# Performance work log

Hardware: AMD Instinct MI355X
Metric: run time of the kernel (lower is better)

The kernel has to match this reference:

```python
import jax, jax.numpy as jnp
import numpy as np


def setup_inputs() -> dict:
    key = jax.random.key(0)
    kq, kk, kv = jax.random.split(key, 3)
    B, S, D = 16, 2048, 128
    q = jax.random.normal(kq, (B, S, D), dtype=jnp.float32)
    k = jax.random.normal(kk, (B, S, D), dtype=jnp.float32)
    v = jax.random.normal(kv, (B, S, D), dtype=jnp.float32)
    return {"q": q, "k": k, "v": v}


def reference(q, k, v):
    # scores = q @ k^T * scale  (scale = 1/sqrt(head_dim), the standard value
    # passed to this module; dropout=0.0 and attn_mask=None per defaults)
    scale = q.shape[-1] ** -0.5
    scores = jnp.einsum('bqd,bkd->bqk', q, k) * scale  # [B, S, S]
    attention = jax.nn.softmax(scores, axis=-1)
    context = jnp.einsum('bqk,bkd->bqd', attention, v)  # [B, S, D]
    return (context, attention)
```

## Files before the change

kernel.cpp:

```cpp
#include <hip/hip_runtime.h>

#define SS 2048
#define DD 128
#define NB 16
#define TM 128
#define TN 64
#define NITER (SS / TN)
#define SCALE 0.08838834764831845f

typedef short bf16x8 __attribute__((ext_vector_type(8)));
typedef float f32x4 __attribute__((ext_vector_type(4)));

#define KSTRIDE 136
#define VSTRIDE 72
#define PSTRIDE 72

__device__ __forceinline__ unsigned short f2bf(float x) {
    unsigned u = __builtin_bit_cast(unsigned, x);
    u += 0x7fffu + ((u >> 16) & 1u);
    return (unsigned short)(u >> 16);
}
__device__ __forceinline__ float bf2f(unsigned short h) {
    unsigned u = ((unsigned)h) << 16;
    return __builtin_bit_cast(float, u);
}

__global__ void cvt_qk_kernel(const float* __restrict__ q, const float* __restrict__ k,
                              unsigned short* __restrict__ qb, unsigned short* __restrict__ kb) {
    int i = (blockIdx.x * 256 + threadIdx.x) * 4;
    float4 a = *(const float4*)(q + i);
    float4 b = *(const float4*)(k + i);
    ushort4 ua; ua.x = f2bf(a.x); ua.y = f2bf(a.y); ua.z = f2bf(a.z); ua.w = f2bf(a.w);
    ushort4 ub; ub.x = f2bf(b.x); ub.y = f2bf(b.y); ub.z = f2bf(b.z); ub.w = f2bf(b.w);
    *(ushort4*)(qb + i) = ua;
    *(ushort4*)(kb + i) = ub;
}

__global__ void tr_v_kernel(const float* __restrict__ v, unsigned short* __restrict__ vt) {
    __shared__ unsigned short t[64 * 72];
    int b = blockIdx.z, sb = blockIdx.y * 64, db = blockIdx.x * 64;
    int tid = threadIdx.x;
    int r16 = tid >> 4, c4 = (tid & 15) * 4;
    for (int i = 0; i < 4; ++i) {
        int sl = i * 16 + r16;
        float4 x = *(const float4*)(v + ((size_t)(b * SS + sb + sl) * DD + db + c4));
        ushort4 u; u.x = f2bf(x.x); u.y = f2bf(x.y); u.z = f2bf(x.z); u.w = f2bf(x.w);
        *(ushort4*)&t[sl * 72 + c4] = u;
    }
    __syncthreads();
    for (int i = 0; i < 4; ++i) {
        int dl = i * 16 + r16;
        ushort4 u;
        u.x = t[(c4 + 0) * 72 + dl];
        u.y = t[(c4 + 1) * 72 + dl];
        u.z = t[(c4 + 2) * 72 + dl];
        u.w = t[(c4 + 3) * 72 + dl];
        *(ushort4*)(vt + ((size_t)(b * DD + db + dl) * SS + sb + c4)) = u;
    }
}

__global__ __launch_bounds__(512, 2)
void attn_kernel(const unsigned short* __restrict__ qb,
                 const unsigned short* __restrict__ kb,
                 const unsigned short* __restrict__ vt,
                 float* __restrict__ attn, float* __restrict__ ctx) {
    __shared__ unsigned short K_lds[TN * KSTRIDE];
    __shared__ unsigned short V_lds[DD * VSTRIDE];
    __shared__ unsigned short P_lds[TM * PSTRIDE];
    __shared__ float rs_lds[TM];
    __shared__ float inv_lds[TM];

    const int tid = threadIdx.x;
    const int lane = tid & 63, w = tid >> 6;
    const int wm = w >> 2, wn = w & 3;
    const int l15 = lane & 15, quad = lane >> 4;
    const int bb = blockIdx.y;
    const int q0 = blockIdx.x * TM;

    if (tid < TM) rs_lds[tid] = 0.0f;

    bf16x8 qf[4][4];
    {
        const unsigned short* qg = qb + ((size_t)(bb * SS + q0 + wm * 64 + l15)) * DD + quad * 8;
        for (int mi = 0; mi < 4; ++mi)
            for (int kk = 0; kk < 4; ++kk)
                qf[mi][kk] = *(const bf16x8*)(qg + mi * 16 * DD + kk * 32);
    }

    const unsigned short* kgb = kb + (size_t)bb * SS * DD;
    const unsigned short* vgb = vt + (size_t)bb * DD * SS;

    float rs[16];
    for (int j = 0; j < 16; ++j) rs[j] = 0.0f;

    for (int it = 0; it < NITER; ++it) {
        const int k0 = it * TN;
        __syncthreads();
        {
            const unsigned short* kg = kgb + (size_t)k0 * DD;
            for (int c = 0; c < 2; ++c) {
                int e = c * 4096 + tid * 8;
                *(bf16x8*)&K_lds[(e >> 7) * KSTRIDE + (e & 127)] = *(const bf16x8*)(kg + e);
            }
        }
        __syncthreads();
        f32x4 acc[4];
        for (int mi = 0; mi < 4; ++mi) acc[mi] = (f32x4){0.f, 0.f, 0.f, 0.f};
        for (int kk = 0; kk < 4; ++kk) {
            bf16x8 bf = *(const bf16x8*)&K_lds[(wn * 16 + l15) * KSTRIDE + kk * 32 + quad * 8];
            for (int mi = 0; mi < 4; ++mi)
                acc[mi] = __builtin_amdgcn_mfma_f32_16x16x32_bf16(qf[mi][kk], bf, acc[mi], 0, 0, 0);
        }
        for (int mi = 0; mi < 4; ++mi)
            for (int r = 0; r < 4; ++r)
                rs[mi * 4 + r] += __expf(acc[mi][r] * SCALE);
    }

    for (int j = 0; j < 16; ++j) {
        float v = rs[j];
        v += __shfl_xor(v, 1, 64);
        v += __shfl_xor(v, 2, 64);
        v += __shfl_xor(v, 4, 64);
        v += __shfl_xor(v, 8, 64);
        rs[j] = v;
    }
    if (l15 == 0)
        for (int mi = 0; mi < 4; ++mi)
            for (int r = 0; r < 4; ++r)
                atomicAdd(&rs_lds[wm * 64 + mi * 16 + quad * 4 + r], rs[mi * 4 + r]);
    __syncthreads();
    if (tid < TM) inv_lds[tid] = 1.0f / rs_lds[tid];
    __syncthreads();
    float inv[16];
    for (int mi = 0; mi < 4; ++mi)
        for (int r = 0; r < 4; ++r)
            inv[mi * 4 + r] = inv_lds[wm * 64 + mi * 16 + quad * 4 + r];

    f32x4 cacc[4][2];
    for (int mi = 0; mi < 4; ++mi)
        for (int ni = 0; ni < 2; ++ni) cacc[mi][ni] = (f32x4){0.f, 0.f, 0.f, 0.f};

    float* ag = attn + (size_t)bb * SS * SS + (size_t)q0 * SS;

    for (int it = 0; it < NITER; ++it) {
        const int k0 = it * TN;
        __syncthreads();
        {
            const unsigned short* kg = kgb + (size_t)k0 * DD;
            for (int c = 0; c < 2; ++c) {
                int e = c * 4096 + tid * 8;
                *(bf16x8*)&K_lds[(e >> 7) * KSTRIDE + (e & 127)] = *(const bf16x8*)(kg + e);
            }
        }
        {
            const unsigned short* vg = vgb + k0;
            for (int c = 0; c < 2; ++c) {
                int e = c * 4096 + tid * 8;
                int dr = e >> 6, ck = e & 63;
                *(bf16x8*)&V_lds[dr * VSTRIDE + ck] = *(const bf16x8*)(vg + (size_t)dr * SS + ck);
            }
        }
        __syncthreads();

        f32x4 acc[4];
        for (int mi = 0; mi < 4; ++mi) acc[mi] = (f32x4){0.f, 0.f, 0.f, 0.f};
        for (int kk = 0; kk < 4; ++kk) {
            bf16x8 bf = *(const bf16x8*)&K_lds[(wn * 16 + l15) * KSTRIDE + kk * 32 + quad * 8];
            for (int mi = 0; mi < 4; ++mi)
                acc[mi] = __builtin_amdgcn_mfma_f32_16x16x32_bf16(qf[mi][kk], bf, acc[mi], 0, 0, 0);
        }
        for (int mi = 0; mi < 4; ++mi)
            for (int r = 0; r < 4; ++r) {
                float p = __expf(acc[mi][r] * SCALE) * inv[mi * 4 + r];
                P_lds[(wm * 64 + mi * 16 + quad * 4 + r) * PSTRIDE + wn * 16 + l15] = f2bf(p);
            }
        __syncthreads();

        for (int kk = 0; kk < 2; ++kk) {
            bf16x8 af[4];
            for (int mi = 0; mi < 4; ++mi)
                af[mi] = *(const bf16x8*)&P_lds[(wm * 64 + mi * 16 + l15) * PSTRIDE + kk * 32 + quad * 8];
            for (int ni = 0; ni < 2; ++ni) {
                bf16x8 bf = *(const bf16x8*)&V_lds[((w & 3) * 32 + ni * 16 + l15) * VSTRIDE + kk * 32 + quad * 8];
                for (int mi = 0; mi < 4; ++mi)
                    cacc[mi][ni] = __builtin_amdgcn_mfma_f32_16x16x32_bf16(af[mi], bf, cacc[mi][ni], 0, 0, 0);
            }
        }

        for (int c = 0; c < 4; ++c) {
            int e = c * 2048 + tid * 4;
            int row = e >> 6, col = e & 63;
            const unsigned short* ps = &P_lds[row * PSTRIDE + col];
            float4 o;
            o.x = bf2f(ps[0]); o.y = bf2f(ps[1]); o.z = bf2f(ps[2]); o.w = bf2f(ps[3]);
            *(float4*)(ag + (size_t)row * SS + k0 + col) = o;
        }
    }

    float* cg = ctx + ((size_t)(bb * SS) + q0) * DD;
    for (int mi = 0; mi < 4; ++mi)
        for (int ni = 0; ni < 2; ++ni)
            for (int r = 0; r < 4; ++r) {
                int row = wm * 64 + mi * 16 + quad * 4 + r;
                int col = (w & 3) * 32 + ni * 16 + l15;
                cg[(size_t)row * DD + col] = cacc[mi][ni][r];
            }
}

extern "C" void kernel_launch(void* const* d_in, const int* in_sizes, int n_in,
                              void* d_out, int out_size, void* d_ws, size_t ws_size,
                              hipStream_t stream) {
    const float* q = (const float*)d_in[0];
    const float* k = (const float*)d_in[1];
    const float* v = (const float*)d_in[2];
    float* ctx = (float*)d_out;
    float* attn = ctx + (size_t)NB * SS * DD;

    unsigned short* qb = (unsigned short*)d_ws;
    unsigned short* kb = qb + (size_t)NB * SS * DD;
    unsigned short* vt = kb + (size_t)NB * SS * DD;

    cvt_qk_kernel<<<dim3((NB * SS * DD) / (256 * 4)), 256, 0, stream>>>(q, k, qb, kb);
    tr_v_kernel<<<dim3(DD / 64, SS / 64, NB), 256, 0, stream>>>(v, vt);
    attn_kernel<<<dim3(SS / TM, NB), 512, 0, stream>>>(qb, kb, vt, attn, ctx);
}
```

Before: 409.8 us.

## Halve query tile, fuse prep kernels, store attention directly from registers

Reduces the query tile from 128 to 64 rows, giving twice as many blocks with higher occupancy bounds, and remaps block IDs to interleave batches. The Q conversion is folded into the attention kernel, and the K conversion and V transpose are merged into one prep kernel. Attention probabilities are now written to global memory straight from registers in full fp32 rather than being re-read from bf16 LDS, and exp is computed via exp2 with a prescaled constant. The trade-off is that K and V are reloaded twice as often per query row, and the per-lane scalar global stores are less coalesced than the previous float4 stores.

After: 371.8 us. -9.3%, faster.

```diff
diff --git a/kernel.cpp b/kernel.cpp
--- a/kernel.cpp
+++ b/kernel.cpp
@@ -3,10 +3,9 @@
 #define SS 2048
 #define DD 128
 #define NB 16
-#define TM 128
+#define TM 64
 #define TN 64
 #define NITER (SS / TN)
-#define SCALE 0.08838834764831845f
 
 typedef short bf16x8 __attribute__((ext_vector_type(8)));
 typedef float f32x4 __attribute__((ext_vector_type(4)));
@@ -14,53 +13,62 @@
 #define KSTRIDE 136
 #define VSTRIDE 72
 #define PSTRIDE 72
+
+#define SL2E (0.08838834764831845f * 1.4426950408889634f)
 
 __device__ __forceinline__ unsigned short f2bf(float x) {
     unsigned u = __builtin_bit_cast(unsigned, x);
     u += 0x7fffu + ((u >> 16) & 1u);
     return (unsigned short)(u >> 16);
 }
-__device__ __forceinline__ float bf2f(unsigned short h) {
-    unsigned u = ((unsigned)h) << 16;
-    return __builtin_bit_cast(float, u);
-}
-
-__global__ void cvt_qk_kernel(const float* __restrict__ q, const float* __restrict__ k,
-                              unsigned short* __restrict__ qb, unsigned short* __restrict__ kb) {
-    int i = (blockIdx.x * 256 + threadIdx.x) * 4;
-    float4 a = *(const float4*)(q + i);
-    float4 b = *(const float4*)(k + i);
-    ushort4 ua; ua.x = f2bf(a.x); ua.y = f2bf(a.y); ua.z = f2bf(a.z); ua.w = f2bf(a.w);
-    ushort4 ub; ub.x = f2bf(b.x); ub.y = f2bf(b.y); ub.z = f2bf(b.z); ub.w = f2bf(b.w);
-    *(ushort4*)(qb + i) = ua;
-    *(ushort4*)(kb + i) = ub;
-}
-
-__global__ void tr_v_kernel(const float* __restrict__ v, unsigned short* __restrict__ vt) {
+
+__device__ __forceinline__ float fexp2(float x) {
+#if __has_builtin(__builtin_amdgcn_exp2f)
+    return __builtin_amdgcn_exp2f(x);
+#else
+    return __expf(x * 0.6931471805599453f);
+#endif
+}
+
+__global__ void prep_kernel(const float* __restrict__ k, const float* __restrict__ v,
+                            unsigned short* __restrict__ kb, unsigned short* __restrict__ vt) {
     __shared__ unsigned short t[64 * 72];
-    int b = blockIdx.z, sb = blockIdx.y * 64, db = blockIdx.x * 64;
-    int tid = threadIdx.x;
-    int r16 = tid >> 4, c4 = (tid & 15) * 4;
-    for (int i = 0; i < 4; ++i) {
-        int sl = i * 16 + r16;
-        float4 x = *(const float4*)(v + ((size_t)(b * SS + sb + sl) * DD + db + c4));
-        ushort4 u; u.x = f2bf(x.x); u.y = f2bf(x.y); u.z = f2bf(x.z); u.w = f2bf(x.w);
-        *(ushort4*)&t[sl * 72 + c4] = u;
-    }
-    __syncthreads();
-    for (int i = 0; i < 4; ++i) {
-        int dl = i * 16 + r16;
-        ushort4 u;
-        u.x = t[(c4 + 0) * 72 + dl];
-        u.y = t[(c4 + 1) * 72 + dl];
-        u.z = t[(c4 + 2) * 72 + dl];
-        u.w = t[(c4 + 3) * 72 + dl];
-        *(ushort4*)(vt + ((size_t)(b * DD + db + dl) * SS + sb + c4)) = u;
-    }
-}
-
-__global__ __launch_bounds__(512, 2)
-void attn_kernel(const unsigned short* __restrict__ qb,
+    const int x = blockIdx.x, b = blockIdx.z, sb = blockIdx.y * 64;
+    const int tid = threadIdx.x;
+    if (x < 2) {
+        const int db = x * 64;
+        const int r16 = tid >> 4, c4 = (tid & 15) * 4;
+        for (int i = 0; i < 4; ++i) {
+            int sl = i * 16 + r16;
+            float4 xx = *(const float4*)(v + ((size_t)(b * SS + sb + sl) * DD + db + c4));
+            ushort4 u; u.x = f2bf(xx.x); u.y = f2bf(xx.y); u.z = f2bf(xx.z); u.w = f2bf(xx.w);
+            *(ushort4*)&t[sl * 72 + c4] = u;
+        }
+        __syncthreads();
+        for (int i = 0; i < 4; ++i) {
+            int dl = i * 16 + r16;
+            ushort4 u;
+            u.x = t[(c4 + 0) * 72 + dl];
+            u.y = t[(c4 + 1) * 72 + dl];
+            u.z = t[(c4 + 2) * 72 + dl];
+            u.w = t[(c4 + 3) * 72 + dl];
+            *(ushort4*)(vt + ((size_t)(b * DD + db + dl) * SS + sb + c4)) = u;
+        }
+    } else {
+        const int c0 = (x - 2) * 64;
+        for (int i = 0; i < 4; ++i) {
+            int e = i * 1024 + tid * 4;
+            int r = e >> 6, c = e & 63;
+            size_t off = (size_t)(b * SS + sb + r) * DD + c0 + c;
+            float4 xx = *(const float4*)(k + off);
+            ushort4 u; u.x = f2bf(xx.x); u.y = f2bf(xx.y); u.z = f2bf(xx.z); u.w = f2bf(xx.w);
+            *(ushort4*)(kb + off) = u;
+        }
+    }
+}
+
+__global__ __launch_bounds__(512, 4)
+void attn_kernel(const float* __restrict__ q,
                  const unsigned short* __restrict__ kb,
                  const unsigned short* __restrict__ vt,
                  float* __restrict__ attn, float* __restrict__ ctx) {
@@ -74,24 +82,88 @@
     const int lane = tid & 63, w = tid >> 6;
     const int wm = w >> 2, wn = w & 3;
     const int l15 = lane & 15, quad = lane >> 4;
-    const int bb = blockIdx.y;
-    const int q0 = blockIdx.x * TM;
+
+    const int bid = blockIdx.x;
+    const int bb = ((bid & 7) << 1) | ((bid >> 3) & 1);
+    const int q0 = (bid >> 4) * TM;
 
     if (tid < TM) rs_lds[tid] = 0.0f;
 
-    bf16x8 qf[4][4];
+    bf16x8 qf[2][4];
     {
-        const unsigned short* qg = qb + ((size_t)(bb * SS + q0 + wm * 64 + l15)) * DD + quad * 8;
-        for (int mi = 0; mi < 4; ++mi)
-            for (int kk = 0; kk < 4; ++kk)
-                qf[mi][kk] = *(const bf16x8*)(qg + mi * 16 * DD + kk * 32);
+        const float* qg = q + ((size_t)(bb * SS + q0 + wm * 32 + l15)) * DD + quad * 8;
+        for (int mi = 0; mi < 2; ++mi)
+            for (int kk = 0; kk < 4; ++kk) {
+                float4 a = *(const float4*)(qg + mi * 16 * DD + kk * 32);
+                float4 b = *(const float4*)(qg + mi * 16 * DD + kk * 32 + 4);
+                bf16x8 f;
+                f[0] = (short)f2bf(a.x); f[1] = (short)f2bf(a.y);
+                f[2] = (short)f2bf(a.z); f[3] = (short)f2bf(a.w);
+                f[4] = (short)f2bf(b.x); f[5] = (short)f2bf(b.y);
+                f[6] = (short)f2bf(b.z); f[7] = (short)f2bf(b.w);
+                qf[mi][kk] = f;
+            }
     }
 
     const unsigned short* kgb = kb + (size_t)bb * SS * DD;
     const unsigned short* vgb = vt + (size_t)bb * DD * SS;
 
-    float rs[16];
-    for (int j = 0; j < 16; ++j) rs[j] = 0.0f;
+    float rs[8];
+    for (int j = 0; j < 8; ++j) rs[j] = 0.0f;
+
+    for (int it = 0; it < NITER; ++it) {
+        __syncthreads();
+        {
+            const unsigned short* kg = kgb + (size_t)(it * TN) * DD;
+            for (int c = 0; c < 2; ++c) {
+                int e = c * 4096 + tid * 8;
+                *(bf16x8*)&K_lds[(e >> 7) * KSTRIDE + (e & 127)] = *(const bf16x8*)(kg + e);
+            }
+        }
+        __syncthreads();
+        f32x4 acc[2];
+        acc[0] = (f32x4){0.f, 0.f, 0.f, 0.f};
+        acc[1] = (f32x4){0.f, 0.f, 0.f, 0.f};
+        for (int kk = 0; kk < 4; ++kk) {
+            bf16x8 bfv = *(const bf16x8*)&K_lds[(wn * 16 + l15) * KSTRIDE + kk * 32 + quad * 8];
+            for (int mi = 0; mi < 2; ++mi)
+                acc[mi] = __builtin_amdgcn_mfma_f32_16x16x32_bf16(qf[mi][kk], bfv, acc[mi], 0, 0, 0);
+        }
+        for (int mi = 0; mi < 2; ++mi)
+            for (int r = 0; r < 4; ++r)
+                rs[mi * 4 + r] += fexp2(acc[mi][r] * SL2E);
+    }
+
+    for (int j = 0; j < 8; ++j) {
+        float s = rs[j];
+        s += __shfl_xor(s, 1, 64);
+        s += __shfl_xor(s, 2, 64);
+        s += __shfl_xor(s, 4, 64);
+        s += __shfl_xor(s, 8, 64);
+        rs[j] = s;
+    }
+    if (l15 == 0)
+        for (int mi = 0; mi < 2; ++mi)
+            for (int r = 0; r < 4; ++r)
+                atomicAdd(&rs_lds[wm * 32 + mi * 16 + quad * 4 + r], rs[mi * 4 + r]);
+    __syncthreads();
+    if (tid < TM) inv_lds[tid] = 1.0f / rs_lds[tid];
+    __syncthreads();
+    float inv[8];
+    for (int mi = 0; mi < 2; ++mi)
+        for (int r = 0; r < 4; ++r)
+            inv[mi * 4 + r] = inv_lds[wm * 32 + mi * 16 + quad * 4 + r];
+
+    f32x4 cacc[2][2];
+    for (int mi = 0; mi < 2; ++mi)
+        for (int ni = 0; ni < 2; ++ni) cacc[mi][ni] = (f32x4){0.f, 0.f, 0.f, 0.f};
+
+    float* ap[8];
+    for (int mi = 0; mi < 2; ++mi)
+        for (int r = 0; r < 4; ++r)
+            ap[mi * 4 + r] = attn + (size_t)bb * SS * SS
+                           + (size_t)(q0 + wm * 32 + mi * 16 + quad * 4 + r) * SS
+                           + wn * 16 + l15;
 
     for (int it = 0; it < NITER; ++it) {
         const int k0 = it * TN;
@@ -102,57 +174,6 @@
                 int e = c * 4096 + tid * 8;
                 *(bf16x8*)&K_lds[(e >> 7) * KSTRIDE + (e & 127)] = *(const bf16x8*)(kg + e);
             }
-        }
-        __syncthreads();
-        f32x4 acc[4];
-        for (int mi = 0; mi < 4; ++mi) acc[mi] = (f32x4){0.f, 0.f, 0.f, 0.f};
-        for (int kk = 0; kk < 4; ++kk) {
-            bf16x8 bf = *(const bf16x8*)&K_lds[(wn * 16 + l15) * KSTRIDE + kk * 32 + quad * 8];
-            for (int mi = 0; mi < 4; ++mi)
-                acc[mi] = __builtin_amdgcn_mfma_f32_16x16x32_bf16(qf[mi][kk], bf, acc[mi], 0, 0, 0);
-        }
-        for (int mi = 0; mi < 4; ++mi)
-            for (int r = 0; r < 4; ++r)
-                rs[mi * 4 + r] += __expf(acc[mi][r] * SCALE);
-    }
-
-    for (int j = 0; j < 16; ++j) {
-        float v = rs[j];
-        v += __shfl_xor(v, 1, 64);
-        v += __shfl_xor(v, 2, 64);
-        v += __shfl_xor(v, 4, 64);
-        v += __shfl_xor(v, 8, 64);
-        rs[j] = v;
-    }
-    if (l15 == 0)
-        for (int mi = 0; mi < 4; ++mi)
-            for (int r = 0; r < 4; ++r)
-                atomicAdd(&rs_lds[wm * 64 + mi * 16 + quad * 4 + r], rs[mi * 4 + r]);
-    __syncthreads();
-    if (tid < TM) inv_lds[tid] = 1.0f / rs_lds[tid];
-    __syncthreads();
-    float inv[16];
-    for (int mi = 0; mi < 4; ++mi)
-        for (int r = 0; r < 4; ++r)
-            inv[mi * 4 + r] = inv_lds[wm * 64 + mi * 16 + quad * 4 + r];
-
-    f32x4 cacc[4][2];
-    for (int mi = 0; mi < 4; ++mi)
-        for (int ni = 0; ni < 2; ++ni) cacc[mi][ni] = (f32x4){0.f, 0.f, 0.f, 0.f};
-
-    float* ag = attn + (size_t)bb * SS * SS + (size_t)q0 * SS;
-
-    for (int it = 0; it < NITER; ++it) {
-        const int k0 = it * TN;
-        __syncthreads();
-        {
-            const unsigned short* kg = kgb + (size_t)k0 * DD;
-            for (int c = 0; c < 2; ++c) {
-                int e = c * 4096 + tid * 8;
-                *(bf16x8*)&K_lds[(e >> 7) * KSTRIDE + (e & 127)] = *(const bf16x8*)(kg + e);
-            }
-        }
-        {
             const unsigned short* vg = vgb + k0;
             for (int c = 0; c < 2; ++c) {
                 int e = c * 4096 + tid * 8;
@@ -162,47 +183,42 @@
         }
         __syncthreads();
 
-        f32x4 acc[4];
-        for (int mi = 0; mi < 4; ++mi) acc[mi] = (f32x4){0.f, 0.f, 0.f, 0.f};
+        f32x4 acc[2];
+        acc[0] = (f32x4){0.f, 0.f, 0.f, 0.f};
+        acc[1] = (f32x4){0.f, 0.f, 0.f, 0.f};
         for (int kk = 0; kk < 4; ++kk) {
-            bf16x8 bf = *(const bf16x8*)&K_lds[(wn * 16 + l15) * KSTRIDE + kk * 32 + quad * 8];
-            for (int mi = 0; mi < 4; ++mi)
-                acc[mi] = __builtin_amdgcn_mfma_f32_16x16x32_bf16(qf[mi][kk], bf, acc[mi], 0, 0, 0);
-        }
-        for (int mi = 0; mi < 4; ++mi)
+            bf16x8 bfv = *(const bf16x8*)&K_lds[(wn * 16 + l15) * KSTRIDE + kk * 32 + quad * 8];
+            for (int mi = 0; mi < 2; ++mi)
+                acc[mi] = __builtin_amdgcn_mfma_f32_16x16x32_bf16(qf[mi][kk], bfv, acc[mi], 0, 0, 0);
+        }
+
+        for (int mi = 0; mi < 2; ++mi)
             for (int r = 0; r < 4; ++r) {
-                float p = __expf(acc[mi][r] * SCALE) * inv[mi * 4 + r];
-                P_lds[(wm * 64 + mi * 16 + quad * 4 + r) * PSTRIDE + wn * 16 + l15] = f2bf(p);
-            }
+                float p = fexp2(acc[mi][r] * SL2E) * inv[mi * 4 + r];
+                ap[mi * 4 + r][0] = p;
+                P_lds[(wm * 32 + mi * 16 + quad * 4 + r) * PSTRIDE + wn * 16 + l15] = f2bf(p);
+            }
+        for (int j = 0; j < 8; ++j) ap[j] += TN;
         __syncthreads();
 
         for (int kk = 0; kk < 2; ++kk) {
-            bf16x8 af[4];
-            for (int mi = 0; mi < 4; ++mi)
-                af[mi] = *(const bf16x8*)&P_lds[(wm * 64 + mi * 16 + l15) * PSTRIDE + kk * 32 + quad * 8];
+            bf16x8 af[2];
+            for (int mi = 0; mi < 2; ++mi)
+                af[mi] = *(const bf16x8*)&P_lds[(wm * 32 + mi * 16 + l15) * PSTRIDE + kk * 32 + quad * 8];
             for (int ni = 0; ni < 2; ++ni) {
-                bf16x8 bf = *(const bf16x8*)&V_lds[((w & 3) * 32 + ni * 16 + l15) * VSTRIDE + kk * 32 + quad * 8];
-                for (int mi = 0; mi < 4; ++mi)
-                    cacc[mi][ni] = __builtin_amdgcn_mfma_f32_16x16x32_bf16(af[mi], bf, cacc[mi][ni], 0, 0, 0);
-            }
-        }
-
-        for (int c = 0; c < 4; ++c) {
-            int e = c * 2048 + tid * 4;
-            int row = e >> 6, col = e & 63;
-            const unsigned short* ps = &P_lds[row * PSTRIDE + col];
-            float4 o;
-            o.x = bf2f(ps[0]); o.y = bf2f(ps[1]); o.z = bf2f(ps[2]); o.w = bf2f(ps[3]);
-            *(float4*)(ag + (size_t)row * SS + k0 + col) = o;
+                bf16x8 bv = *(const bf16x8*)&V_lds[(wn * 32 + ni * 16 + l15) * VSTRIDE + kk * 32 + quad * 8];
+                for (int mi = 0; mi < 2; ++mi)
+                    cacc[mi][ni] = __builtin_amdgcn_mfma_f32_16x16x32_bf16(af[mi], bv, cacc[mi][ni], 0, 0, 0);
+            }
         }
     }
 
     float* cg = ctx + ((size_t)(bb * SS) + q0) * DD;
-    for (int mi = 0; mi < 4; ++mi)
+    for (int mi = 0; mi < 2; ++mi)
         for (int ni = 0; ni < 2; ++ni)
             for (int r = 0; r < 4; ++r) {
-                int row = wm * 64 + mi * 16 + quad * 4 + r;
-                int col = (w & 3) * 32 + ni * 16 + l15;
+                int row = wm * 32 + mi * 16 + quad * 4 + r;
+                int col = wn * 32 + ni * 16 + l15;
                 cg[(size_t)row * DD + col] = cacc[mi][ni][r];
             }
 }
@@ -216,11 +232,9 @@
     float* ctx = (float*)d_out;
     float* attn = ctx + (size_t)NB * SS * DD;
 
-    unsigned short* qb = (unsigned short*)d_ws;
-    unsigned short* kb = qb + (size_t)NB * SS * DD;
+    unsigned short* kb = (unsigned short*)d_ws;
     unsigned short* vt = kb + (size_t)NB * SS * DD;
 
-    cvt_qk_kernel<<<dim3((NB * SS * DD) / (256 * 4)), 256, 0, stream>>>(q, k, qb, kb);
-    tr_v_kernel<<<dim3(DD / 64, SS / 64, NB), 256, 0, stream>>>(v, vt);
-    attn_kernel<<<dim3(SS / TM, NB), 512, 0, stream>>>(qb, kb, vt, attn, ctx);
-}
+    prep_kernel<<<dim3(4, SS / 64, NB), 256, 0, stream>>>(k, v, kb, vt);
+    attn_kernel<<<dim3((SS / TM) * NB), 512, 0, stream>>>(q, kb, vt, attn, ctx);
+}
```
